# Kernel optimization log

Measured on AMD Instinct MI355X. Metric: run time of the kernel, lower is better.

## Reference

```python
import jax, jax.numpy as jnp
import numpy as np

B, IN, H = 16384, 512, 1024

def _linear_params(key, fan_in, fan_out):
    k1, k2 = jax.random.split(key)
    bound = 1.0 / np.sqrt(fan_in)
    W = jax.random.uniform(k1, (fan_out, fan_in), jnp.float32, -bound, bound)
    b = jax.random.uniform(k2, (fan_out,), jnp.float32, -bound, bound)
    return W, b

def setup_inputs() -> dict:
    key = jax.random.key(0)
    ks = jax.random.split(key, 10)
    x = jax.random.normal(ks[0], (B, IN), jnp.float32)
    h_prev = jax.random.normal(ks[1], (B, H), jnp.float32)
    c_prev = jax.random.normal(ks[2], (B, H), jnp.float32)
    W_i, b_i = _linear_params(ks[3], IN + H, H)
    W_f, b_f = _linear_params(ks[4], IN + H, H)
    W_o, b_o = _linear_params(ks[5], IN + H, H)
    W_g, b_g = _linear_params(ks[6], IN + H, H)
    W_a, b_a = _linear_params(ks[7], H, 1)
    W_ht, b_ht = _linear_params(ks[8], IN, H)
    W_hg, b_hg = _linear_params(ks[9], IN, H)
    return dict(x=x, h_prev=h_prev, c_prev=c_prev,
                W_i=W_i, b_i=b_i, W_f=W_f, b_f=b_f, W_o=W_o, b_o=b_o,
                W_g=W_g, b_g=b_g, W_a=W_a, b_a=b_a,
                W_ht=W_ht, b_ht=b_ht, W_hg=W_hg, b_hg=b_hg)

def reference(x, h_prev, c_prev, W_i, b_i, W_f, b_f, W_o, b_o, W_g, b_g,
              W_a, b_a, W_ht, b_ht, W_hg, b_hg):
    combined = jnp.concatenate([x, h_prev], axis=1)  # [B, IN+H]
    # fuse 4 gate GEMMs into one concatenated-weight GEMM
    W_gates = jnp.concatenate([W_i, W_f, W_o, W_g], axis=0)  # [4H, IN+H]
    b_gates = jnp.concatenate([b_i, b_f, b_o, b_g], axis=0)  # [4H]
    gates = combined @ W_gates.T + b_gates                   # [B, 4H]
    i, f, o, g = jnp.split(gates, 4, axis=1)
    i = jax.nn.sigmoid(i)
    f = jax.nn.sigmoid(f)
    o = jax.nn.sigmoid(o)
    g = jnp.tanh(g)
    c = f * c_prev + i * g
    h = o * jnp.tanh(c)
    # attention: softmax over the batch dim (dim=0), logits [B, 1]
    attn_logits = h @ W_a.T + b_a                 # [B, 1]
    attn = jax.nn.softmax(attn_logits, axis=0)    # [B, 1]
    h = h * attn
    # highway merge
    t = x @ W_ht.T + b_ht
    gate = jax.nn.sigmoid(x @ W_hg.T + b_hg)
    h = gate * t + (1.0 - gate) * h
    # dropout in eval mode: identity
    return (h, c)
```

## Files before the change

### kernel.cpp

```cpp
#include <hip/hip_runtime.h>
#include <stdint.h>

#define B_  16384
#define IN_ 512
#define H_  1024
#define KC_ 1536

typedef unsigned short u16;
typedef __attribute__((ext_vector_type(4))) float f32x4;
typedef __attribute__((ext_vector_type(8))) short s16x8;


__device__ __forceinline__ u16 f2bf(float f) {
  union { float f; uint32_t u; } un; un.f = f;
  uint32_t u = un.u;
  uint32_t r = (u + 0x7FFFu + ((u >> 16) & 1u)) >> 16;
  return (u16)r;
}

__device__ __forceinline__ float fast_sigmoid(float x) {
  return 1.f / (1.f + __expf(-x));
}
__device__ __forceinline__ float fast_tanh(float x) {
  return 1.f - 2.f / (1.f + __expf(2.f * x));
}

__device__ __forceinline__ void mfma_bf16(f32x4& d, s16x8 a, s16x8 b) {
  asm("v_mfma_f32_16x16x32_bf16 %0, %1, %2, %0" : "+v"(d) : "v"(a), "v"(b));
}

__device__ __forceinline__ void async_copy16(void* lds, const void* g) {
  __builtin_amdgcn_global_load_lds(
      (const __attribute__((address_space(1))) void*)g,
      (__attribute__((address_space(3))) void*)lds, 16, 0, 0);
}

__global__ __launch_bounds__(256)
void k0_convert(const float* __restrict__ x, const float* __restrict__ hprev,
                const float* __restrict__ Wi, const float* __restrict__ Wf,
                const float* __restrict__ Wo, const float* __restrict__ Wg,
                const float* __restrict__ Wht, const float* __restrict__ Whg,
                u16* __restrict__ comb, u16* __restrict__ wcat,
                u16* __restrict__ wht2, float* __restrict__ sum_slot)
{
  const int NC_COMB = (B_ * KC_) / 4;
  const int NC_WCAT = (4 * H_ * KC_) / 4;
  const int NC_WHT  = (2 * H_ * IN_) / 4;
  const int TOTAL = NC_COMB + NC_WCAT + NC_WHT;
  const int stride = gridDim.x * blockDim.x;

  for (int idx = blockIdx.x * blockDim.x + threadIdx.x; idx < TOTAL; idx += stride) {
    const float* src;
    u16* dst;
    if (idx < NC_COMB) {
      int row = idx / 384, cq = idx % 384;
      src = (cq < 128) ? (x + (size_t)row * IN_ + cq * 4)
                       : (hprev + (size_t)row * H_ + (cq - 128) * 4);
      dst = comb + (size_t)idx * 4;
    } else if (idx < NC_COMB + NC_WCAT) {
      int j = idx - NC_COMB;
      int g = j / 393216;
      int rem = j % 393216;
      const float* W = (g == 0) ? Wi : (g == 1) ? Wf : (g == 2) ? Wo : Wg;
      src = W + (size_t)rem * 4;
      dst = wcat + (size_t)j * 4;
    } else {
      int j = idx - NC_COMB - NC_WCAT;
      int m = j / 131072;
      int rem = j % 131072;
      src = (m ? Whg : Wht) + (size_t)rem * 4;
      dst = wht2 + (size_t)j * 4;
    }
    float4 v = *(const float4*)src;
    uint32_t p0 = (uint32_t)f2bf(v.x) | ((uint32_t)f2bf(v.y) << 16);
    uint32_t p1 = (uint32_t)f2bf(v.z) | ((uint32_t)f2bf(v.w) << 16);
    *(uint2*)dst = make_uint2(p0, p1);
  }
  if (blockIdx.x == 0 && threadIdx.x == 0) sum_slot[0] = 0.f;
}

__global__ __launch_bounds__(256, 2)
void k1_gates(const u16* __restrict__ comb, const u16* __restrict__ wcat,
              const float* __restrict__ bi, const float* __restrict__ bf_,
              const float* __restrict__ bo, const float* __restrict__ bg,
              const float* __restrict__ c_prev,
              float* __restrict__ c_out, float* __restrict__ h_pre)
{
  __shared__ __attribute__((aligned(128))) char lds[32768];
  char* lds_a = lds;
  char* lds_b = lds + 16384;

  const int tid = threadIdx.x;
  const int w = tid >> 6, lane = tid & 63;
  const int lrow = lane & 15, lkg = lane >> 4;
  const int wm = w >> 1, wn = w & 1;
  const int m0 = blockIdx.y * 128;
  const int n0 = blockIdx.x * 32;

  const u16* agp[4]; const u16* bgp[4];
  char* alp[4]; char* blp[4];
#pragma unroll
  for (int t = 0; t < 4; ++t) {
    int j = w * 256 + t * 64 + lane;
    int r = j >> 3, q = j & 7;
    int qs = q ^ (r & 7);
    agp[t] = comb + (size_t)(m0 + r) * KC_ + qs * 8;
    alp[t] = lds_a + (w * 256 + t * 64) * 16;
    int g = (r >> 4) & 3, n = ((r >> 6) << 4) + (r & 15);
    bgp[t] = wcat + ((size_t)(g * H_ + n0 + n)) * KC_ + qs * 8;
    blp[t] = lds_b + (w * 256 + t * 64) * 16;
  }

  f32x4 acc[4][4];
#pragma unroll
  for (int i = 0; i < 4; ++i)
#pragma unroll
    for (int j = 0; j < 4; ++j) acc[i][j] = (f32x4){0.f, 0.f, 0.f, 0.f};

  const int sw = (lrow & 7) << 4;
  int aoff[4], boff[4];
#pragma unroll
  for (int fm = 0; fm < 4; ++fm) aoff[fm] = (wm * 64 + fm * 16 + lrow) * 128;
#pragma unroll
  for (int fc = 0; fc < 4; ++fc) boff[fc] = (wn * 64 + fc * 16 + lrow) * 128;

  for (int kt = 0; kt < KC_ / 64; ++kt) {
#pragma unroll
    for (int t = 0; t < 4; ++t) {
      async_copy16(alp[t], agp[t] + kt * 64);
      async_copy16(blp[t], bgp[t] + kt * 64);
    }
    __syncthreads();
#pragma unroll
    for (int ks = 0; ks < 2; ++ks) {
      const int koff = (ks * 64 + lkg * 16) ^ sw;
      s16x8 a[4], b[4];
#pragma unroll
      for (int fm = 0; fm < 4; ++fm) a[fm] = *(const s16x8*)(lds_a + aoff[fm] + koff);
#pragma unroll
      for (int fc = 0; fc < 4; ++fc) b[fc] = *(const s16x8*)(lds_b + boff[fc] + koff);
#pragma unroll
      for (int fm = 0; fm < 4; ++fm)
#pragma unroll
        for (int fc = 0; fc < 4; ++fc) mfma_bf16(acc[fm][fc], a[fm], b[fc]);
    }
    __syncthreads();
  }

  const int h = n0 + wn * 16 + lrow;
  const float vbi = bi[h], vbf = bf_[h], vbo = bo[h], vbg = bg[h];
#pragma unroll
  for (int fm = 0; fm < 4; ++fm) {
    const int row0 = m0 + wm * 64 + fm * 16 + lkg * 4;
#pragma unroll
    for (int r4 = 0; r4 < 4; ++r4) {
      const size_t off = (size_t)(row0 + r4) * H_ + h;
      float iv = fast_sigmoid(acc[fm][0][r4] + vbi);
      float fv = fast_sigmoid(acc[fm][1][r4] + vbf);
      float ov = fast_sigmoid(acc[fm][2][r4] + vbo);
      float gv = fast_tanh(acc[fm][3][r4] + vbg);
      float c = fv * c_prev[off] + iv * gv;
      c_out[off] = c;
      h_pre[off] = ov * fast_tanh(c);
    }
  }
}

__global__ __launch_bounds__(256)
void k2_softmax(const float* __restrict__ h_pre, const float* __restrict__ Wa,
                const float* __restrict__ ba, float* __restrict__ e,
                float* __restrict__ sum_slot)
{
  __shared__ float wsum[4];
  const int w = threadIdx.x >> 6, lane = threadIdx.x & 63;
  const int r = blockIdx.x * 4 + w;
  const float4* hp = (const float4*)(h_pre + (size_t)r * H_);
  const float4* wa = (const float4*)Wa;
  float s = 0.f;
#pragma unroll
  for (int j = 0; j < 4; ++j) {
    float4 hv = hp[lane * 4 + j];
    float4 wv = wa[lane * 4 + j];
    s += hv.x * wv.x + hv.y * wv.y + hv.z * wv.z + hv.w * wv.w;
  }
#pragma unroll
  for (int off = 32; off; off >>= 1) s += __shfl_xor(s, off);
  float ev = __expf(s + ba[0]);
  if (lane == 0) { e[r] = ev; wsum[w] = ev; }
  __syncthreads();
  if (threadIdx.x == 0) atomicAdd(sum_slot, wsum[0] + wsum[1] + wsum[2] + wsum[3]);
}

__global__ __launch_bounds__(256, 2)
void k3_highway(const u16* __restrict__ comb, const u16* __restrict__ wht2,
                const float* __restrict__ bht, const float* __restrict__ bhg,
                const float* __restrict__ e, const float* __restrict__ sum_slot,
                float* __restrict__ h_out)
{
  __shared__ __attribute__((aligned(128))) char lds[32768];
  char* lds_a = lds;
  char* lds_b = lds + 16384;

  const int tid = threadIdx.x;
  const int w = tid >> 6, lane = tid & 63;
  const int lrow = lane & 15, lkg = lane >> 4;
  const int wm = w >> 1, wn = w & 1;
  const int m0 = blockIdx.y * 128;
  const int h0 = blockIdx.x * 64;

  const u16* agp[4]; const u16* bgp[4];
  char* alp[4]; char* blp[4];
#pragma unroll
  for (int t = 0; t < 4; ++t) {
    int j = w * 256 + t * 64 + lane;
    int r = j >> 3, q = j & 7;
    int qs = q ^ (r & 7);
    agp[t] = comb + (size_t)(m0 + r) * KC_ + qs * 8;
    alp[t] = lds_a + (w * 256 + t * 64) * 16;
    int mat = (r >> 4) & 1, n = ((r >> 5) << 4) + (r & 15);
    bgp[t] = wht2 + ((size_t)(mat * H_ + h0 + n)) * IN_ + qs * 8;
    blp[t] = lds_b + (w * 256 + t * 64) * 16;
  }

  f32x4 acc[4][4];
#pragma unroll
  for (int i = 0; i < 4; ++i)
#pragma unroll
    for (int j = 0; j < 4; ++j) acc[i][j] = (f32x4){0.f, 0.f, 0.f, 0.f};

  const int sw = (lrow & 7) << 4;
  int aoff[4], boff[4];
#pragma unroll
  for (int fm = 0; fm < 4; ++fm) aoff[fm] = (wm * 64 + fm * 16 + lrow) * 128;
#pragma unroll
  for (int fc = 0; fc < 4; ++fc) boff[fc] = (wn * 64 + fc * 16 + lrow) * 128;

  for (int kt = 0; kt < IN_ / 64; ++kt) {
#pragma unroll
    for (int t = 0; t < 4; ++t) {
      async_copy16(alp[t], agp[t] + kt * 64);
      async_copy16(blp[t], bgp[t] + kt * 64);
    }
    __syncthreads();
#pragma unroll
    for (int ks = 0; ks < 2; ++ks) {
      const int koff = (ks * 64 + lkg * 16) ^ sw;
      s16x8 a[4], b[4];
#pragma unroll
      for (int fm = 0; fm < 4; ++fm) a[fm] = *(const s16x8*)(lds_a + aoff[fm] + koff);
#pragma unroll
      for (int fc = 0; fc < 4; ++fc) b[fc] = *(const s16x8*)(lds_b + boff[fc] + koff);
#pragma unroll
      for (int fm = 0; fm < 4; ++fm)
#pragma unroll
        for (int fc = 0; fc < 4; ++fc) mfma_bf16(acc[fm][fc], a[fm], b[fc]);
    }
    __syncthreads();
  }

  const float invs = 1.f / sum_slot[0];
  const int hA = h0 + wn * 32 + lrow;
  const float vbht0 = bht[hA], vbht1 = bht[hA + 16];
  const float vbhg0 = bhg[hA], vbhg1 = bhg[hA + 16];
#pragma unroll
  for (int fm = 0; fm < 4; ++fm) {
    const int row0 = m0 + wm * 64 + fm * 16 + lkg * 4;
#pragma unroll
    for (int r4 = 0; r4 < 4; ++r4) {
      const int row = row0 + r4;
      const float escale = e[row] * invs;
#pragma unroll
      for (int hc = 0; hc < 2; ++hc) {
        const int h = hA + hc * 16;
        const size_t off = (size_t)row * H_ + h;
        float tv = acc[fm][2 * hc][r4] + (hc ? vbht1 : vbht0);
        float gv = fast_sigmoid(acc[fm][2 * hc + 1][r4] + (hc ? vbhg1 : vbhg0));
        float ha = h_out[off] * escale;
        h_out[off] = gv * tv + (1.f - gv) * ha;
      }
    }
  }
}

extern "C" void kernel_launch(void* const* d_in, const int* in_sizes, int n_in,
                              void* d_out, int out_size, void* d_ws, size_t ws_size,
                              hipStream_t stream) {
  const float* x      = (const float*)d_in[0];
  const float* h_prev = (const float*)d_in[1];
  const float* c_prev = (const float*)d_in[2];
  const float* Wi  = (const float*)d_in[3];
  const float* bi  = (const float*)d_in[4];
  const float* Wf  = (const float*)d_in[5];
  const float* bf_ = (const float*)d_in[6];
  const float* Wo  = (const float*)d_in[7];
  const float* bo  = (const float*)d_in[8];
  const float* Wg  = (const float*)d_in[9];
  const float* bg  = (const float*)d_in[10];
  const float* Wa  = (const float*)d_in[11];
  const float* ba  = (const float*)d_in[12];
  const float* Wht = (const float*)d_in[13];
  const float* bht = (const float*)d_in[14];
  const float* Whg = (const float*)d_in[15];
  const float* bhg = (const float*)d_in[16];

  char* ws = (char*)d_ws;
  float* sum_slot = (float*)(ws + 0);
  float* e        = (float*)(ws + 256);
  u16* comb = (u16*)(ws + 65792);
  u16* wcat = (u16*)(ws + 50397440);
  u16* wht2 = (u16*)(ws + 62980352);

  float* h_out = (float*)d_out;
  float* c_out = (float*)d_out + (size_t)B_ * H_;

  hipLaunchKernelGGL(k0_convert, dim3(2048), dim3(256), 0, stream,
                     x, h_prev, Wi, Wf, Wo, Wg, Wht, Whg, comb, wcat, wht2, sum_slot);
  hipLaunchKernelGGL(k1_gates, dim3(H_ / 32, B_ / 128), dim3(256), 0, stream,
                     comb, wcat, bi, bf_, bo, bg, c_prev, c_out, h_out);
  hipLaunchKernelGGL(k2_softmax, dim3(B_ / 4), dim3(256), 0, stream,
                     h_out, Wa, ba, e, sum_slot);
  hipLaunchKernelGGL(k3_highway, dim3(H_ / 64, B_ / 128), dim3(256), 0, stream,
                     comb, wht2, bht, bhg, e, sum_slot, h_out);
}
```

Baseline: 573.7 us.

## Rewrite gate GEMM as 256x256 double-buffered pipelined kernel with grid swizzle

Replaces the 128x128-tile gate GEMM with a 512-thread kernel using 256x(4x64) tiles, 128 KB of double-buffered LDS, staggered async prefetch of the next A and the B after that, s_barrier/waitcnt phase scheduling, setprio around MFMAs and a block-index swizzle for L2 locality. This is meant to overlap global loads with MFMA work and raise data reuse in the dominant GEMM. Separately, the atomic softmax sum is replaced by per-block partials plus a single-block reduction kernel, which adds a launch but removes atomics. The large LDS footprint and hand-tuned waitcnt counts limit occupancy and risk subtle ordering bugs.

```diff
diff --git a/kernel.cpp b/kernel.cpp
--- a/kernel.cpp
+++ b/kernel.cpp
@@ -26,7 +26,7 @@
 }
 
 __device__ __forceinline__ void mfma_bf16(f32x4& d, s16x8 a, s16x8 b) {
-  asm("v_mfma_f32_16x16x32_bf16 %0, %1, %2, %0" : "+v"(d) : "v"(a), "v"(b));
+  asm volatile("v_mfma_f32_16x16x32_bf16 %0, %1, %2, %0" : "+v"(d) : "v"(a), "v"(b));
 }
 
 __device__ __forceinline__ void async_copy16(void* lds, const void* g) {
@@ -41,7 +41,7 @@
                 const float* __restrict__ Wo, const float* __restrict__ Wg,
                 const float* __restrict__ Wht, const float* __restrict__ Whg,
                 u16* __restrict__ comb, u16* __restrict__ wcat,
-                u16* __restrict__ wht2, float* __restrict__ sum_slot)
+                u16* __restrict__ wht2)
 {
   const int NC_COMB = (B_ * KC_) / 4;
   const int NC_WCAT = (4 * H_ * KC_) / 4;
@@ -76,89 +76,150 @@
     uint32_t p1 = (uint32_t)f2bf(v.z) | ((uint32_t)f2bf(v.w) << 16);
     *(uint2*)dst = make_uint2(p0, p1);
   }
-  if (blockIdx.x == 0 && threadIdx.x == 0) sum_slot[0] = 0.f;
-}
-
-__global__ __launch_bounds__(256, 2)
-void k1_gates(const u16* __restrict__ comb, const u16* __restrict__ wcat,
-              const float* __restrict__ bi, const float* __restrict__ bf_,
-              const float* __restrict__ bo, const float* __restrict__ bg,
-              const float* __restrict__ c_prev,
-              float* __restrict__ c_out, float* __restrict__ h_pre)
+}
+
+__global__ __launch_bounds__(512, 2)
+void k1_gates8ph(const u16* __restrict__ comb, const u16* __restrict__ wcat,
+                 const float* __restrict__ bi, const float* __restrict__ bf_,
+                 const float* __restrict__ bo, const float* __restrict__ bg,
+                 const float* __restrict__ c_prev,
+                 float* __restrict__ c_out, float* __restrict__ h_pre)
 {
-  __shared__ __attribute__((aligned(128))) char lds[32768];
-  char* lds_a = lds;
-  char* lds_b = lds + 16384;
+  __shared__ __attribute__((aligned(128))) char lds[131072];
 
   const int tid = threadIdx.x;
   const int w = tid >> 6, lane = tid & 63;
   const int lrow = lane & 15, lkg = lane >> 4;
-  const int wm = w >> 1, wn = w & 1;
-  const int m0 = blockIdx.y * 128;
-  const int n0 = blockIdx.x * 32;
-
-  const u16* agp[4]; const u16* bgp[4];
-  char* alp[4]; char* blp[4];
-#pragma unroll
-  for (int t = 0; t < 4; ++t) {
-    int j = w * 256 + t * 64 + lane;
-    int r = j >> 3, q = j & 7;
-    int qs = q ^ (r & 7);
-    agp[t] = comb + (size_t)(m0 + r) * KC_ + qs * 8;
-    alp[t] = lds_a + (w * 256 + t * 64) * 16;
-    int g = (r >> 4) & 3, n = ((r >> 6) << 4) + (r & 15);
-    bgp[t] = wcat + ((size_t)(g * H_ + n0 + n)) * KC_ + qs * 8;
-    blp[t] = lds_b + (w * 256 + t * 64) * 16;
-  }
-
-  f32x4 acc[4][4];
-#pragma unroll
-  for (int i = 0; i < 4; ++i)
+  const int wm = w >> 2, wn = w & 3;
+
+  int bid = blockIdx.y * gridDim.x + blockIdx.x;
+  int swz = (bid & 7) * 128 + (bid >> 3);
+  const int bx = swz & 15, by = swz >> 4;
+  const int m0 = by * 256, n0h = bx * 64;
+
+  const u16* pA[2][2]; const u16* pB[2][2];
+  int ldsA[2][2], ldsB[2][2];
+#pragma unroll
+  for (int h = 0; h < 2; ++h)
+#pragma unroll
+    for (int t = 0; t < 2; ++t) {
+      int i = w * 128 + t * 64 + lane;
+      int rh = i >> 3, c = i & 7;
+      int cs = c ^ (rh & 7);
+      int rt = h * 128 + rh;
+      pA[h][t] = comb + (size_t)(m0 + rt) * KC_ + cs * 8;
+      int g = (rt >> 4) & 3, hc = n0h + ((rt >> 6) << 4) + (rt & 15);
+      pB[h][t] = wcat + ((size_t)(g * H_ + hc)) * KC_ + cs * 8;
+      ldsA[h][t] = h * 16384 + (w * 128 + t * 64) * 16;
+      ldsB[h][t] = 32768 + h * 16384 + (w * 128 + t * 64) * 16;
+    }
+
+  int aoff[8], boff[4], kx[2];
+#pragma unroll
+  for (int mr = 0; mr < 8; ++mr) aoff[mr] = (wm * 128 + mr * 16 + lrow) * 128;
+#pragma unroll
+  for (int fc = 0; fc < 4; ++fc) boff[fc] = 32768 + (wn * 64 + fc * 16 + lrow) * 128;
+  kx[0] = ((lkg) ^ (lrow & 7)) << 4;
+  kx[1] = ((4 + lkg) ^ (lrow & 7)) << 4;
+
+  f32x4 acc[8][4];
+#pragma unroll
+  for (int i = 0; i < 8; ++i)
 #pragma unroll
     for (int j = 0; j < 4; ++j) acc[i][j] = (f32x4){0.f, 0.f, 0.f, 0.f};
 
-  const int sw = (lrow & 7) << 4;
-  int aoff[4], boff[4];
-#pragma unroll
-  for (int fm = 0; fm < 4; ++fm) aoff[fm] = (wm * 64 + fm * 16 + lrow) * 128;
-#pragma unroll
-  for (int fc = 0; fc < 4; ++fc) boff[fc] = (wn * 64 + fc * 16 + lrow) * 128;
-
-  for (int kt = 0; kt < KC_ / 64; ++kt) {
-#pragma unroll
-    for (int t = 0; t < 4; ++t) {
-      async_copy16(alp[t], agp[t] + kt * 64);
-      async_copy16(blp[t], bgp[t] + kt * 64);
-    }
-    __syncthreads();
-#pragma unroll
-    for (int ks = 0; ks < 2; ++ks) {
-      const int koff = (ks * 64 + lkg * 16) ^ sw;
-      s16x8 a[4], b[4];
-#pragma unroll
-      for (int fm = 0; fm < 4; ++fm) a[fm] = *(const s16x8*)(lds_a + aoff[fm] + koff);
-#pragma unroll
-      for (int fc = 0; fc < 4; ++fc) b[fc] = *(const s16x8*)(lds_b + boff[fc] + koff);
-#pragma unroll
-      for (int fm = 0; fm < 4; ++fm)
-#pragma unroll
-        for (int fc = 0; fc < 4; ++fc) mfma_bf16(acc[fm][fc], a[fm], b[fc]);
-    }
-    __syncthreads();
-  }
-
-  const int h = n0 + wn * 16 + lrow;
-  const float vbi = bi[h], vbf = bf_[h], vbo = bo[h], vbg = bg[h];
-#pragma unroll
-  for (int fm = 0; fm < 4; ++fm) {
-    const int row0 = m0 + wm * 64 + fm * 16 + lkg * 4;
+  {
+    char* b0 = lds;
+    char* b1 = lds + 65536;
+#pragma unroll
+    for (int h = 0; h < 2; ++h)
+#pragma unroll
+      for (int t = 0; t < 2; ++t) async_copy16(b0 + ldsA[h][t], pA[h][t]);
+#pragma unroll
+    for (int h = 0; h < 2; ++h)
+#pragma unroll
+      for (int t = 0; t < 2; ++t) async_copy16(b0 + ldsB[h][t], pB[h][t]);
+#pragma unroll
+    for (int h = 0; h < 2; ++h)
+#pragma unroll
+      for (int t = 0; t < 2; ++t) async_copy16(b1 + ldsB[h][t], pB[h][t] + 64);
+    asm volatile("s_waitcnt vmcnt(4)" ::: "memory");
+    __builtin_amdgcn_sched_barrier(0);
+    __builtin_amdgcn_s_barrier();
+  }
+
+  for (int S = 0; S < 24; ++S) {
+    const int cur = S & 1;
+    char* bufc = lds + cur * 65536;
+    char* bufo = lds + (cur ^ 1) * 65536;
+    s16x8 bfr[4][2];
+#pragma unroll
+    for (int q = 0; q < 4; ++q) {
+      s16x8 afr[2][2];
+#pragma unroll
+      for (int j = 0; j < 2; ++j)
+#pragma unroll
+        for (int kk = 0; kk < 2; ++kk)
+          afr[j][kk] = *(const s16x8*)(bufc + aoff[2 * q + j] + kx[kk]);
+      if (q == 0) {
+#pragma unroll
+        for (int fc = 0; fc < 4; ++fc)
+#pragma unroll
+          for (int kk = 0; kk < 2; ++kk)
+            bfr[fc][kk] = *(const s16x8*)(bufc + boff[fc] + kx[kk]);
+      }
+      if (q == 0 && S < 23) {
+        async_copy16(bufo + ldsA[0][0], pA[0][0] + (S + 1) * 64);
+        async_copy16(bufo + ldsA[0][1], pA[0][1] + (S + 1) * 64);
+      }
+      if (q == 1 && S < 23) {
+        async_copy16(bufo + ldsA[1][0], pA[1][0] + (S + 1) * 64);
+        async_copy16(bufo + ldsA[1][1], pA[1][1] + (S + 1) * 64);
+      }
+      if (q == 2 && S < 22) {
+        async_copy16(bufc + ldsB[0][0], pB[0][0] + (S + 2) * 64);
+        async_copy16(bufc + ldsB[0][1], pB[0][1] + (S + 2) * 64);
+      }
+      if (q == 3 && S < 22) {
+        async_copy16(bufc + ldsB[1][0], pB[1][0] + (S + 2) * 64);
+        async_copy16(bufc + ldsB[1][1], pB[1][1] + (S + 2) * 64);
+      }
+      asm volatile("" ::: "memory");
+      __builtin_amdgcn_sched_barrier(0);
+      __builtin_amdgcn_s_barrier();
+      asm volatile("s_waitcnt lgkmcnt(0)" ::: "memory");
+      __builtin_amdgcn_sched_barrier(0);
+      __builtin_amdgcn_s_setprio(1);
+#pragma unroll
+      for (int kk = 0; kk < 2; ++kk)
+#pragma unroll
+        for (int fc = 0; fc < 4; ++fc)
+#pragma unroll
+          for (int j = 0; j < 2; ++j)
+            mfma_bf16(acc[2 * q + j][fc], afr[j][kk], bfr[fc][kk]);
+      __builtin_amdgcn_s_setprio(0);
+      if (q == 3) {
+        if (S < 22) asm volatile("s_waitcnt vmcnt(4)" ::: "memory");
+        else        asm volatile("s_waitcnt vmcnt(0)" ::: "memory");
+      }
+      asm volatile("" ::: "memory");
+      __builtin_amdgcn_sched_barrier(0);
+      __builtin_amdgcn_s_barrier();
+    }
+  }
+
+  const int hcol = n0h + wn * 16 + lrow;
+  const float vbi = bi[hcol], vbf = bf_[hcol], vbo = bo[hcol], vbg = bg[hcol];
+#pragma unroll
+  for (int mr = 0; mr < 8; ++mr) {
+    const int row0 = m0 + wm * 128 + mr * 16 + lkg * 4;
 #pragma unroll
     for (int r4 = 0; r4 < 4; ++r4) {
-      const size_t off = (size_t)(row0 + r4) * H_ + h;
-      float iv = fast_sigmoid(acc[fm][0][r4] + vbi);
-      float fv = fast_sigmoid(acc[fm][1][r4] + vbf);
-      float ov = fast_sigmoid(acc[fm][2][r4] + vbo);
-      float gv = fast_tanh(acc[fm][3][r4] + vbg);
+      const size_t off = (size_t)(row0 + r4) * H_ + hcol;
+      float iv = fast_sigmoid(acc[mr][0][r4] + vbi);
+      float fv = fast_sigmoid(acc[mr][1][r4] + vbf);
+      float ov = fast_sigmoid(acc[mr][2][r4] + vbo);
+      float gv = fast_tanh(acc[mr][3][r4] + vbg);
       float c = fv * c_prev[off] + iv * gv;
       c_out[off] = c;
       h_pre[off] = ov * fast_tanh(c);
@@ -167,9 +228,9 @@
 }
 
 __global__ __launch_bounds__(256)
-void k2_softmax(const float* __restrict__ h_pre, const float* __restrict__ Wa,
-                const float* __restrict__ ba, float* __restrict__ e,
-                float* __restrict__ sum_slot)
+void k2_logits(const float* __restrict__ h_pre, const float* __restrict__ Wa,
+               const float* __restrict__ ba, float* __restrict__ e,
+               float* __restrict__ partial)
 {
   __shared__ float wsum[4];
   const int w = threadIdx.x >> 6, lane = threadIdx.x & 63;
@@ -188,7 +249,20 @@
   float ev = __expf(s + ba[0]);
   if (lane == 0) { e[r] = ev; wsum[w] = ev; }
   __syncthreads();
-  if (threadIdx.x == 0) atomicAdd(sum_slot, wsum[0] + wsum[1] + wsum[2] + wsum[3]);
+  if (threadIdx.x == 0) partial[blockIdx.x] = wsum[0] + wsum[1] + wsum[2] + wsum[3];
+}
+
+__global__ __launch_bounds__(256)
+void k2_reduce(const float* __restrict__ partial, float* __restrict__ sum_slot)
+{
+  __shared__ float ws4[4];
+  float s = 0.f;
+  for (int i = threadIdx.x; i < 4096; i += 256) s += partial[i];
+#pragma unroll
+  for (int off = 32; off; off >>= 1) s += __shfl_xor(s, off);
+  if ((threadIdx.x & 63) == 0) ws4[threadIdx.x >> 6] = s;
+  __syncthreads();
+  if (threadIdx.x == 0) sum_slot[0] = ws4[0] + ws4[1] + ws4[2] + ws4[3];
 }
 
 __global__ __launch_bounds__(256, 2)
@@ -309,16 +383,19 @@
   u16* comb = (u16*)(ws + 65792);
   u16* wcat = (u16*)(ws + 50397440);
   u16* wht2 = (u16*)(ws + 62980352);
+  float* partial = (float*)(ws + 65077504);
 
   float* h_out = (float*)d_out;
   float* c_out = (float*)d_out + (size_t)B_ * H_;
 
   hipLaunchKernelGGL(k0_convert, dim3(2048), dim3(256), 0, stream,
-                     x, h_prev, Wi, Wf, Wo, Wg, Wht, Whg, comb, wcat, wht2, sum_slot);
-  hipLaunchKernelGGL(k1_gates, dim3(H_ / 32, B_ / 128), dim3(256), 0, stream,
+                     x, h_prev, Wi, Wf, Wo, Wg, Wht, Whg, comb, wcat, wht2);
+  hipLaunchKernelGGL(k1_gates8ph, dim3(16, 64), dim3(512), 0, stream,
                      comb, wcat, bi, bf_, bo, bg, c_prev, c_out, h_out);
-  hipLaunchKernelGGL(k2_softmax, dim3(B_ / 4), dim3(256), 0, stream,
-                     h_out, Wa, ba, e, sum_slot);
+  hipLaunchKernelGGL(k2_logits, dim3(B_ / 4), dim3(256), 0, stream,
+                     h_out, Wa, ba, e, partial);
+  hipLaunchKernelGGL(k2_reduce, dim3(1), dim3(256), 0, stream,
+                     partial, sum_slot);
   hipLaunchKernelGGL(k3_highway, dim3(H_ / 64, B_ / 128), dim3(256), 0, stream,
                      comb, wht2, bht, bhg, e, sum_slot, h_out);
 }
```

Result: faster. 532.1 us (-7.3%).

## Fuse attention logit dot product into gates epilogue and drop atomic sum

Applied to the files above, without the earlier changes.

The gates kernel epilogue now multiplies each h value by the attention weight and reduces across lanes and waves, writing per-block partial logits. This removes the softmax kernel's full re-read of the 64MB h_pre buffer. The softmax kernel then sums 32 partials per row, exponentiates, and writes per-block partial sums instead of doing an atomicAdd, and the highway kernel reduces the 64 partial sums itself. The cost is extra shuffles, an LDS round-trip and a block barrier in the GEMM epilogue, plus a small partial-logit buffer. The mfma asm is also marked volatile.

```diff
diff --git a/kernel.cpp b/kernel.cpp
--- a/kernel.cpp
+++ b/kernel.cpp
@@ -26,7 +26,7 @@
 }
 
 __device__ __forceinline__ void mfma_bf16(f32x4& d, s16x8 a, s16x8 b) {
-  asm("v_mfma_f32_16x16x32_bf16 %0, %1, %2, %0" : "+v"(d) : "v"(a), "v"(b));
+  asm volatile("v_mfma_f32_16x16x32_bf16 %0, %1, %2, %0" : "+v"(d) : "v"(a), "v"(b));
 }
 
 __device__ __forceinline__ void async_copy16(void* lds, const void* g) {
@@ -41,7 +41,7 @@
                 const float* __restrict__ Wo, const float* __restrict__ Wg,
                 const float* __restrict__ Wht, const float* __restrict__ Whg,
                 u16* __restrict__ comb, u16* __restrict__ wcat,
-                u16* __restrict__ wht2, float* __restrict__ sum_slot)
+                u16* __restrict__ wht2)
 {
   const int NC_COMB = (B_ * KC_) / 4;
   const int NC_WCAT = (4 * H_ * KC_) / 4;
@@ -76,15 +76,15 @@
     uint32_t p1 = (uint32_t)f2bf(v.z) | ((uint32_t)f2bf(v.w) << 16);
     *(uint2*)dst = make_uint2(p0, p1);
   }
-  if (blockIdx.x == 0 && threadIdx.x == 0) sum_slot[0] = 0.f;
 }
 
 __global__ __launch_bounds__(256, 2)
 void k1_gates(const u16* __restrict__ comb, const u16* __restrict__ wcat,
               const float* __restrict__ bi, const float* __restrict__ bf_,
               const float* __restrict__ bo, const float* __restrict__ bg,
-              const float* __restrict__ c_prev,
-              float* __restrict__ c_out, float* __restrict__ h_pre)
+              const float* __restrict__ c_prev, const float* __restrict__ Wa,
+              float* __restrict__ c_out, float* __restrict__ h_pre,
+              float* __restrict__ partial_logit)
 {
   __shared__ __attribute__((aligned(128))) char lds[32768];
   char* lds_a = lds;
@@ -149,6 +149,8 @@
 
   const int h = n0 + wn * 16 + lrow;
   const float vbi = bi[h], vbf = bf_[h], vbo = bo[h], vbg = bg[h];
+  const float wa_h = Wa[h];
+  float slog[4][4];
 #pragma unroll
   for (int fm = 0; fm < 4; ++fm) {
     const int row0 = m0 + wm * 64 + fm * 16 + lkg * 4;
@@ -161,40 +163,56 @@
       float gv = fast_tanh(acc[fm][3][r4] + vbg);
       float c = fv * c_prev[off] + iv * gv;
       c_out[off] = c;
-      h_pre[off] = ov * fast_tanh(c);
-    }
-  }
+      float hv = ov * fast_tanh(c);
+      h_pre[off] = hv;
+      slog[fm][r4] = hv * wa_h;
+    }
+  }
+#pragma unroll
+  for (int fm = 0; fm < 4; ++fm)
+#pragma unroll
+    for (int r4 = 0; r4 < 4; ++r4) {
+#pragma unroll
+      for (int st = 1; st < 16; st <<= 1)
+        slog[fm][r4] += __shfl_xor(slog[fm][r4], st);
+    }
+  float* part = (float*)lds;
+  if (lrow == 0) {
+#pragma unroll
+    for (int fm = 0; fm < 4; ++fm)
+#pragma unroll
+      for (int r4 = 0; r4 < 4; ++r4)
+        part[wn * 128 + wm * 64 + fm * 16 + lkg * 4 + r4] = slog[fm][r4];
+  }
+  __syncthreads();
+  if (tid < 128)
+    partial_logit[(size_t)blockIdx.x * B_ + m0 + tid] = part[tid] + part[128 + tid];
 }
 
 __global__ __launch_bounds__(256)
-void k2_softmax(const float* __restrict__ h_pre, const float* __restrict__ Wa,
-                const float* __restrict__ ba, float* __restrict__ e,
-                float* __restrict__ sum_slot)
+void k2_expsum(const float* __restrict__ partial_logit, const float* __restrict__ ba,
+               float* __restrict__ e, float* __restrict__ psum)
 {
-  __shared__ float wsum[4];
+  __shared__ float ws4[4];
+  const int r = blockIdx.x * 256 + threadIdx.x;
   const int w = threadIdx.x >> 6, lane = threadIdx.x & 63;
-  const int r = blockIdx.x * 4 + w;
-  const float4* hp = (const float4*)(h_pre + (size_t)r * H_);
-  const float4* wa = (const float4*)Wa;
   float s = 0.f;
 #pragma unroll
-  for (int j = 0; j < 4; ++j) {
-    float4 hv = hp[lane * 4 + j];
-    float4 wv = wa[lane * 4 + j];
-    s += hv.x * wv.x + hv.y * wv.y + hv.z * wv.z + hv.w * wv.w;
-  }
-#pragma unroll
-  for (int off = 32; off; off >>= 1) s += __shfl_xor(s, off);
+  for (int p = 0; p < 32; ++p) s += partial_logit[(size_t)p * B_ + r];
   float ev = __expf(s + ba[0]);
-  if (lane == 0) { e[r] = ev; wsum[w] = ev; }
+  e[r] = ev;
+  float t = ev;
+#pragma unroll
+  for (int off = 32; off; off >>= 1) t += __shfl_xor(t, off);
+  if (lane == 0) ws4[w] = t;
   __syncthreads();
-  if (threadIdx.x == 0) atomicAdd(sum_slot, wsum[0] + wsum[1] + wsum[2] + wsum[3]);
+  if (threadIdx.x == 0) psum[blockIdx.x] = ws4[0] + ws4[1] + ws4[2] + ws4[3];
 }
 
 __global__ __launch_bounds__(256, 2)
 void k3_highway(const u16* __restrict__ comb, const u16* __restrict__ wht2,
                 const float* __restrict__ bht, const float* __restrict__ bhg,
-                const float* __restrict__ e, const float* __restrict__ sum_slot,
+                const float* __restrict__ e, const float* __restrict__ psum,
                 float* __restrict__ h_out)
 {
   __shared__ __attribute__((aligned(128))) char lds[32768];
@@ -258,7 +276,11 @@
     __syncthreads();
   }
 
-  const float invs = 1.f / sum_slot[0];
+  float sv = psum[lane];
+#pragma unroll
+  for (int off = 32; off; off >>= 1) sv += __shfl_xor(sv, off);
+  const float invs = 1.f / sv;
+
   const int hA = h0 + wn * 32 + lrow;
   const float vbht0 = bht[hA], vbht1 = bht[hA + 16];
   const float vbhg0 = bhg[hA], vbhg1 = bhg[hA + 16];
@@ -304,21 +326,22 @@
   const float* bhg = (const float*)d_in[16];
 
   char* ws = (char*)d_ws;
-  float* sum_slot = (float*)(ws + 0);
-  float* e        = (float*)(ws + 256);
+  float* psum = (float*)(ws + 0);
+  float* e    = (float*)(ws + 256);
   u16* comb = (u16*)(ws + 65792);
   u16* wcat = (u16*)(ws + 50397440);
   u16* wht2 = (u16*)(ws + 62980352);
+  float* partial_logit = (float*)(ws + 65077504);
 
   float* h_out = (float*)d_out;
   float* c_out = (float*)d_out + (size_t)B_ * H_;
 
   hipLaunchKernelGGL(k0_convert, dim3(2048), dim3(256), 0, stream,
-                     x, h_prev, Wi, Wf, Wo, Wg, Wht, Whg, comb, wcat, wht2, sum_slot);
+                     x, h_prev, Wi, Wf, Wo, Wg, Wht, Whg, comb, wcat, wht2);
   hipLaunchKernelGGL(k1_gates, dim3(H_ / 32, B_ / 128), dim3(256), 0, stream,
-                     comb, wcat, bi, bf_, bo, bg, c_prev, c_out, h_out);
-  hipLaunchKernelGGL(k2_softmax, dim3(B_ / 4), dim3(256), 0, stream,
-                     h_out, Wa, ba, e, sum_slot);
+                     comb, wcat, bi, bf_, bo, bg, c_prev, Wa, c_out, h_out, partial_logit);
+  hipLaunchKernelGGL(k2_expsum, dim3(B_ / 256), dim3(256), 0, stream,
+                     partial_logit, ba, e, psum);
   hipLaunchKernelGGL(k3_highway, dim3(H_ / 64, B_ / 128), dim3(256), 0, stream,
-                     comb, wht2, bht, bhg, e, sum_slot, h_out);
-}
+                     comb, wht2, bht, bhg, e, psum, h_out);
+}
```

New measurement: 536.0 us. 6.6% less time.
